# Optimization experiments

Hardware: AMD Instinct MI355X
Metric: run time of the kernel (lower is better)

The kernel has to match this reference:

```python
import jax, jax.numpy as jnp
import numpy as np

N_LAYERS = 4
D_MODEL = 64        # 8*8 hardcoded in source
D_STATE = 128
D_CONV = 4
EXPAND = 2
HEADDIM = 64        # Mamba2Simple default
D_INNER = EXPAND * D_MODEL            # 128
NHEADS = D_INNER // HEADDIM           # 2
NGROUPS = 1
D_IN_PROJ = 2 * D_INNER + 2 * NGROUPS * D_STATE + NHEADS   # 514
CONV_DIM = D_INNER + 2 * NGROUPS * D_STATE                 # 384
EPS = 1e-5
B_SZ, SEQ = 8, 4096


def setup_inputs() -> dict:
    key = jax.random.key(0)
    ks = jax.random.split(key, 8)
    s = 0.02
    x = jax.random.normal(ks[0], (B_SZ, SEQ, D_MODEL), jnp.float32)
    in_proj_w = jax.random.normal(ks[1], (N_LAYERS, D_IN_PROJ, D_MODEL), jnp.float32) * s
    conv_w = jax.random.normal(ks[2], (N_LAYERS, CONV_DIM, 1, D_CONV), jnp.float32) * 0.2
    conv_b = jnp.zeros((N_LAYERS, CONV_DIM), jnp.float32)
    # dt_bias ~ inverse-softplus of small dt values
    dt_bias = jax.random.uniform(ks[3], (N_LAYERS, NHEADS), jnp.float32, -4.0, 0.0)
    A_log = jnp.log(jax.random.uniform(ks[4], (N_LAYERS, NHEADS), jnp.float32, 1.0, 16.0))
    D = jnp.ones((N_LAYERS, NHEADS), jnp.float32)
    norm_w = jnp.ones((N_LAYERS, D_INNER), jnp.float32)
    out_proj_w = jax.random.normal(ks[5], (N_LAYERS, D_MODEL, D_INNER), jnp.float32) * s
    return {"x": x, "in_proj_w": in_proj_w, "conv_w": conv_w, "conv_b": conv_b,
            "dt_bias": dt_bias, "A_log": A_log, "D": D, "norm_w": norm_w,
            "out_proj_w": out_proj_w}


def _ssm(xh, dt, A, Bm, Cm):
    """Selective-scan SSM. xh:(B,L,H,P) dt:(B,L,H) A:(H,) Bm,Cm:(B,L,S) -> (B,L,H,P)"""
    dA = jnp.exp(dt * A)  # (B,L,H)

    def step(h, inp):
        dA_t, dt_t, x_t, B_t, C_t = inp
        # h: (B,H,P,S)
        h = h * dA_t[:, :, None, None] + (dt_t[:, :, None] * x_t)[..., None] * B_t[:, None, None, :]
        y = jnp.einsum('bhps,bs->bhp', h, C_t)
        return h, y

    b = xh.shape[0]
    h0 = jnp.zeros((b, NHEADS, HEADDIM, D_STATE), xh.dtype)
    xs = (jnp.moveaxis(dA, 1, 0), jnp.moveaxis(dt, 1, 0), jnp.moveaxis(xh, 1, 0),
          jnp.moveaxis(Bm, 1, 0), jnp.moveaxis(Cm, 1, 0))
    _, ys = jax.lax.scan(step, h0, xs)
    return jnp.moveaxis(ys, 0, 1)


def _layer(x, p):
    in_w, cw, cb, dtb, Alog, Dp, nw, ow = p
    zxbcdt = x @ in_w.T                                   # (B,L,514)
    z = zxbcdt[..., :D_INNER]
    xBC = zxbcdt[..., D_INNER:D_INNER + CONV_DIM]
    dt = jax.nn.softplus(zxbcdt[..., -NHEADS:] + dtb)     # (B,L,H)
    # causal depthwise conv over sequence
    xc = jnp.moveaxis(xBC, -1, 1)                         # (B,C,L)
    xc = jax.lax.conv_general_dilated(xc, cw, (1,), [(D_CONV - 1, 0)],
                                      dimension_numbers=('NCH', 'OIH', 'NCH'),
                                      feature_group_count=CONV_DIM)
    xBC = jax.nn.silu(jnp.moveaxis(xc + cb[None, :, None], 1, -1))
    xs = xBC[..., :D_INNER]
    Bm = xBC[..., D_INNER:D_INNER + D_STATE]
    Cm = xBC[..., D_INNER + D_STATE:]
    xh = xs.reshape(xs.shape[0], xs.shape[1], NHEADS, HEADDIM)
    A = -jnp.exp(Alog)                                    # (H,)
    y = _ssm(xh, dt, A, Bm, Cm) + Dp[None, None, :, None] * xh
    y = y.reshape(y.shape[0], y.shape[1], D_INNER)
    # gated RMSNorm (norm_before_gate=False): rmsnorm(y * silu(z)) * w
    y = y * jax.nn.silu(z)
    y = y * jax.lax.rsqrt(jnp.mean(y * y, axis=-1, keepdims=True) + EPS) * nw
    return y @ ow.T


def reference(x, in_proj_w, conv_w, conv_b, dt_bias, A_log, D, norm_w, out_proj_w):
    def body(xc, p):
        return _layer(xc, p) + xc, None
    out, _ = jax.lax.scan(body, x, (in_proj_w, conv_w, conv_b, dt_bias, A_log, D, norm_w, out_proj_w))
    return out
```

## Files before the change

kernel.cpp:

```cpp
#include <hip/hip_runtime.h>
#include <math.h>

#define B_SZ 8
#define SEQ  4096
#define DM   64
#define DI   128
#define NH   2
#define HD   64
#define DS   128
#define DIP  514
#define XW   384
#define CD   384
#define QC   64
#define NC   64
#define NR   (B_SZ*SEQ)
#define WPAD 576

typedef __attribute__((ext_vector_type(8))) short bf16x8;
typedef __attribute__((ext_vector_type(4))) float f32x4;

__device__ __forceinline__ unsigned short f2bf(float f) {
    union { float f; unsigned int u; } x; x.f = f;
    unsigned int r = x.u + 0x7fffu + ((x.u >> 16) & 1u);
    return (unsigned short)(r >> 16);
}
__device__ __forceinline__ float bf2f(unsigned short h) {
    union { unsigned int u; float f; } x; x.u = ((unsigned int)h) << 16;
    return x.f;
}
__device__ __forceinline__ bf16x8 fragld(const unsigned short* base, int r0, int k0, int ld) {
    int l = threadIdx.x & 63;
    return *(const bf16x8*)(base + (ptrdiff_t)(r0 + (l & 15)) * ld + k0 + (l >> 4) * 8);
}

__global__ __launch_bounds__(256) void k_wcvt(const float* __restrict__ in_w,
                                              const float* __restrict__ out_w,
                                              unsigned short* __restrict__ Wb,
                                              unsigned short* __restrict__ OWb) {
    int idx = blockIdx.x * 256 + threadIdx.x;
    if (idx < 4 * WPAD * 64) {
        int l = idx / (WPAD * 64), r = idx % (WPAD * 64);
        int n = r >> 6, k = r & 63;
        float v = (n < DIP) ? in_w[(size_t)l * DIP * 64 + (size_t)n * 64 + k] : 0.f;
        Wb[idx] = f2bf(v);
    }
    if (idx < 4 * 64 * 128) OWb[idx] = f2bf(out_w[idx]);
}

__global__ __launch_bounds__(256) void k_xcvt(const float* __restrict__ X,
                                              unsigned short* __restrict__ Xb) {
    int idx = (blockIdx.x * 256 + threadIdx.x) * 4;
    float4 v = *(const float4*)(X + idx);
    uint2 p;
    p.x = f2bf(v.x) | ((unsigned int)f2bf(v.y) << 16);
    p.y = f2bf(v.z) | ((unsigned int)f2bf(v.w) << 16);
    *(uint2*)(Xb + idx) = p;
}

__global__ __launch_bounds__(256) void k_inproj(const unsigned short* __restrict__ Xb,
                                                const unsigned short* __restrict__ Wb,
                                                unsigned short* __restrict__ ZXb,
                                                float* __restrict__ DT) {
    int m0 = blockIdx.x * 256;
    int ny = blockIdx.y;
    int tid = threadIdx.x;
    int wid = tid >> 6, lane = tid & 63;
    int q4 = lane >> 4, c16 = lane & 15;
    int mb = m0 + wid * 64;
    bf16x8 af[4][2];
#pragma unroll
    for (int mt = 0; mt < 4; mt++)
#pragma unroll
        for (int ks = 0; ks < 2; ks++)
            af[mt][ks] = *(const bf16x8*)(Xb + (size_t)(mb + mt * 16 + c16) * 64 + ks * 32 + q4 * 8);
    if (ny < 6) {
#pragma unroll
        for (int nt = 0; nt < 4; nt++) {
            bf16x8 bf[2];
#pragma unroll
            for (int ks = 0; ks < 2; ks++)
                bf[ks] = *(const bf16x8*)(Wb + (size_t)(128 + ny * 64 + nt * 16 + c16) * 64 + ks * 32 + q4 * 8);
#pragma unroll
            for (int mt = 0; mt < 4; mt++) {
                f32x4 acc = {0.f, 0.f, 0.f, 0.f};
                acc = __builtin_amdgcn_mfma_f32_16x16x32_bf16(af[mt][0], bf[0], acc, 0, 0, 0);
                acc = __builtin_amdgcn_mfma_f32_16x16x32_bf16(af[mt][1], bf[1], acc, 0, 0, 0);
#pragma unroll
                for (int rr = 0; rr < 4; rr++) {
                    float v = acc[rr];
                    float vn = __shfl_xor(v, 1);
                    if (!(lane & 1)) {
                        unsigned int pk = f2bf(v) | ((unsigned int)f2bf(vn) << 16);
                        *(unsigned int*)(ZXb + (size_t)(mb + mt * 16 + q4 * 4 + rr) * XW + ny * 64 + nt * 16 + c16) = pk;
                    }
                }
            }
        }
    } else {
        bf16x8 bf[2];
#pragma unroll
        for (int ks = 0; ks < 2; ks++)
            bf[ks] = *(const bf16x8*)(Wb + (size_t)(512 + c16) * 64 + ks * 32 + q4 * 8);
#pragma unroll
        for (int mt = 0; mt < 4; mt++) {
            f32x4 acc = {0.f, 0.f, 0.f, 0.f};
            acc = __builtin_amdgcn_mfma_f32_16x16x32_bf16(af[mt][0], bf[0], acc, 0, 0, 0);
            acc = __builtin_amdgcn_mfma_f32_16x16x32_bf16(af[mt][1], bf[1], acc, 0, 0, 0);
            if (c16 < 2)
#pragma unroll
                for (int rr = 0; rr < 4; rr++)
                    DT[(size_t)(mb + mt * 16 + q4 * 4 + rr) * 2 + c16] = acc[rr];
        }
    }
}

__global__ __launch_bounds__(1024, 8) void k_chunk1(
        const unsigned short* __restrict__ ZXb, const float* __restrict__ DT,
        const float* __restrict__ CW, const float* __restrict__ CB,
        const float* __restrict__ dtb, const float* __restrict__ Alog,
        const float* __restrict__ Dv,
        unsigned short* __restrict__ SL, unsigned short* __restrict__ CBuf,
        float* __restrict__ EB,
        float* __restrict__ TB, unsigned short* __restrict__ YBb) {
    __shared__ unsigned short sBt[128][72];
    __shared__ unsigned short sXt[128][72];
    __shared__ unsigned short uBC[2][64][136];
    __shared__ float s_cum[2][64], s_dt[2][64], s_w[2][64];
    unsigned short (*sM)[64][72] = (unsigned short (*)[64][72])&uBC[0][0][0];

    int c = blockIdx.x, b = blockIdx.y;
    size_t rbase = (size_t)b * SEQ + c * QC;
    int tid = threadIdx.x;
    int wid = tid >> 6, lane = tid & 63;
    int q4 = lane >> 4, c16 = lane & 15;

    if (wid < 2) {
        int h = wid, j = lane;
        float raw = DT[(rbase + j) * 2 + h] + dtb[h];
        float dt = (raw > 20.f) ? raw : log1pf(__expf(raw));
        float A = -__expf(Alog[h]);
        float x = dt * A;
        for (int off = 1; off < 64; off <<= 1) {
            float o = __shfl_up(x, off);
            if (lane >= off) x += o;
        }
        float T = __shfl(x, 63);
        s_dt[h][j] = dt;
        s_cum[h][j] = x;
        s_w[h][j] = __expf(T - x) * dt;
        EB[((size_t)(b * NC + c)) * 128 + h * 64 + j] = __expf(x);
        if (j == 0) TB[(b * 2 + h) * NC + c] = __expf(T);
    }

    size_t cbbase = ((size_t)(b * NC + c)) * 8192;
    for (int e = tid; e < 64 * 96; e += 1024) {
        int j = e / 96;
        int q = e - j * 96;
        int cc = q * 4;
        int l = c * QC + j;
        const unsigned short* zp = ZXb + (rbase + j) * XW + cc;
        uint2 a0 = *(const uint2*)zp;
        uint2 a1 = make_uint2(0, 0), a2 = make_uint2(0, 0), a3 = make_uint2(0, 0);
        if (l >= 1) a1 = *(const uint2*)(zp - XW);
        if (l >= 2) a2 = *(const uint2*)(zp - 2 * XW);
        if (l >= 3) a3 = *(const uint2*)(zp - 3 * XW);
        float v[4];
#pragma unroll
        for (int u = 0; u < 4; u++) {
            unsigned int w0 = (u < 2) ? a0.x : a0.y;
            unsigned int w1 = (u < 2) ? a1.x : a1.y;
            unsigned int w2 = (u < 2) ? a2.x : a2.y;
            unsigned int w3 = (u < 2) ? a3.x : a3.y;
            int sh = (u & 1) * 16;
            float r0 = bf2f((unsigned short)(w0 >> sh));
            float r1 = bf2f((unsigned short)(w1 >> sh));
            float r2 = bf2f((unsigned short)(w2 >> sh));
            float r3 = bf2f((unsigned short)(w3 >> sh));
            float4 wv = *(const float4*)(CW + (cc + u) * 4);
            float tt = CB[cc + u] + wv.w * r0 + wv.z * r1 + wv.y * r2 + wv.x * r3;
            v[u] = tt / (1.f + __expf(-tt));
        }
        if (cc < 128) {
#pragma unroll
            for (int u = 0; u < 4; u++) sXt[cc + u][j] = f2bf(v[u]);
        } else if (cc < 256) {
            int s = cc - 128;
            unsigned int p0 = f2bf(v[0]) | ((unsigned int)f2bf(v[1]) << 16);
            unsigned int p1 = f2bf(v[2]) | ((unsigned int)f2bf(v[3]) << 16);
            *(uint2*)&uBC[0][j][s] = make_uint2(p0, p1);
#pragma unroll
            for (int u = 0; u < 4; u++) sBt[s + u][j] = f2bf(v[u]);
        } else {
            int s = cc - 256;
            unsigned int p0 = f2bf(v[0]) | ((unsigned int)f2bf(v[1]) << 16);
            unsigned int p1 = f2bf(v[2]) | ((unsigned int)f2bf(v[3]) << 16);
            *(uint2*)&uBC[1][j][s] = make_uint2(p0, p1);
            *(uint2*)(CBuf + cbbase + (size_t)j * 128 + s) = make_uint2(p0, p1);
        }
    }
    __syncthreads();

    f32x4 gacc;
    {
        int it = wid >> 2, jt = wid & 3;
        f32x4 acc = {0.f, 0.f, 0.f, 0.f};
        for (int ks = 0; ks < 4; ks++) {
            bf16x8 a = fragld(&uBC[1][0][0], it * 16, ks * 32, 136);
            bf16x8 bb = fragld(&uBC[0][0][0], jt * 16, ks * 32, 136);
            acc = __builtin_amdgcn_mfma_f32_16x16x32_bf16(a, bb, acc, 0, 0, 0);
        }
        gacc = acc;
    }
    __syncthreads();
    {
        int it = wid >> 2, jt = wid & 3;
        int j = jt * 16 + c16;
        for (int rr = 0; rr < 4; rr++) {
            int i = it * 16 + q4 * 4 + rr;
            float gv = gacc[rr];
            for (int h = 0; h < 2; h++) {
                float m = 0.f;
                if (j <= i) m = gv * __expf(s_cum[h][i] - s_cum[h][j]) * s_dt[h][j];
                sM[h][i][j] = f2bf(m);
            }
        }
    }
    __syncthreads();

    size_t ybase = ((size_t)(b * NC + c)) * 8192;
#pragma unroll
    for (int u = 0; u < 2; u++) {
        int idx = wid * 2 + u;
        int h = idx >> 4, tt = idx & 15;
        int it = tt >> 2, pt = tt & 3;
        float dco = Dv[h];
        int pg = h * 64 + pt * 16 + c16;
        f32x4 acc;
        for (int rr = 0; rr < 4; rr++) {
            int i = it * 16 + q4 * 4 + rr;
            acc[rr] = dco * bf2f(sXt[pg][i]);
        }
        for (int ks = 0; ks < 2; ks++) {
            bf16x8 a = fragld(&sM[h][0][0], it * 16, ks * 32, 72);
            bf16x8 bb = fragld(&sXt[0][0], h * 64 + pt * 16, ks * 32, 72);
            acc = __builtin_amdgcn_mfma_f32_16x16x32_bf16(a, bb, acc, 0, 0, 0);
        }
        uint2 pk;
        pk.x = f2bf(acc[0]) | ((unsigned int)f2bf(acc[1]) << 16);
        pk.y = f2bf(acc[2]) | ((unsigned int)f2bf(acc[3]) << 16);
        *(uint2*)(YBb + ybase + (size_t)idx * 256 + lane * 4) = pk;
    }
    size_t slbase = ((size_t)(b * NC + c)) * 16384;
#pragma unroll
    for (int u = 0; u < 4; u++) {
        int idx = wid * 4 + u;
        int ptl = idx >> 3, st = idx & 7;
        int h = ptl >> 2;
        f32x4 acc = {0.f, 0.f, 0.f, 0.f};
        for (int ks = 0; ks < 2; ks++) {
            int jb = ks * 32 + (lane >> 4) * 8;
            bf16x8 a = fragld(&sXt[0][0], ptl * 16, ks * 32, 72);
            bf16x8 aw;
#pragma unroll
            for (int t = 0; t < 8; t++) aw[t] = (short)f2bf(bf2f((unsigned short)a[t]) * s_w[h][jb + t]);
            bf16x8 bb = fragld(&sBt[0][0], st * 16, ks * 32, 72);
            acc = __builtin_amdgcn_mfma_f32_16x16x32_bf16(aw, bb, acc, 0, 0, 0);
        }
        int s = st * 16 + c16;
        for (int rr = 0; rr < 4; rr++) {
            int p = ptl * 16 + q4 * 4 + rr;
            float vv = acc[rr];
            float vn = __shfl_xor(vv, 1);
            if (!(lane & 1)) {
                unsigned int pk = f2bf(vv) | ((unsigned int)f2bf(vn) << 16);
                *(unsigned int*)(SL + slbase + (size_t)p * 128 + s) = pk;
            }
        }
    }
}

__global__ __launch_bounds__(256) void k_scan(unsigned short* __restrict__ SL,
                                              const float* __restrict__ TB) {
    int bid = blockIdx.x;
    int b = bid >> 6;
    int ps = (bid & 63) * 256 + threadIdx.x;
    int h = ps >> 13;
    const float* dAp = TB + (b * 2 + h) * NC;
    size_t base = (size_t)(b * NC) * 16384 + ps;
    float hacc = 0.f;
#pragma unroll 8
    for (int cc = 0; cc < NC; cc++) {
        size_t idx = base + (size_t)cc * 16384;
        float slv = bf2f(SL[idx]);
        SL[idx] = f2bf(hacc);
        hacc = hacc * dAp[cc] + slv;
    }
}

__global__ __launch_bounds__(1024, 8) void k_fused(
        const unsigned short* __restrict__ SL, const unsigned short* __restrict__ CBuf,
        const float* __restrict__ EB,
        const unsigned short* __restrict__ YBb, const unsigned short* __restrict__ Wzb,
        const float* __restrict__ NW, const unsigned short* __restrict__ OWb,
        unsigned short* __restrict__ Xb, float* __restrict__ OutF,
        const unsigned short* __restrict__ WbN,
        unsigned short* __restrict__ ZXbO,
        float* __restrict__ DTO,
        int last) {
    __shared__ __attribute__((aligned(16))) unsigned short sH[128][136];
    __shared__ __attribute__((aligned(16))) unsigned short sE[128][136];
    float* sGf = (float*)&sH[0][0];
    unsigned short (*sG)[136] = (unsigned short (*)[136])&sE[0][0];
    unsigned short (*sX2)[72] = (unsigned short (*)[72])&sH[0][0];

    int c = blockIdx.x, b = blockIdx.y;
    size_t rbase = (size_t)b * SEQ + c * QC;
    int tid = threadIdx.x;
    int wid = tid >> 6, lane = tid & 63;
    size_t base = ((size_t)(b * NC + c)) * 16384;
    for (int u = 0; u < 2; u++) {
        int e = u * 1024 + tid;
        int row = e >> 4, cb8 = (e & 15) * 8;
        *(uint4*)&sH[row][cb8] = *(const uint4*)(SL + base + (size_t)row * 128 + cb8);
    }
    size_t cbbase = ((size_t)(b * NC + c)) * 8192;
    size_t ebase  = ((size_t)(b * NC + c)) * 128;
    {
        int i = tid >> 4, sc = (tid & 15) * 8;
        uint4 cv = *(const uint4*)(CBuf + cbbase + (size_t)i * 128 + sc);
        float e0 = EB[ebase + i], e1 = EB[ebase + 64 + i];
        unsigned int w[4] = {cv.x, cv.y, cv.z, cv.w};
        uint4 o0, o1;
        unsigned int* po0 = &o0.x;
        unsigned int* po1 = &o1.x;
#pragma unroll
        for (int t = 0; t < 4; t++) {
            float lo = bf2f((unsigned short)(w[t] & 0xffff));
            float hi = bf2f((unsigned short)(w[t] >> 16));
            po0[t] = f2bf(lo * e0) | ((unsigned int)f2bf(hi * e0) << 16);
            po1[t] = f2bf(lo * e1) | ((unsigned int)f2bf(hi * e1) << 16);
        }
        *(uint4*)&sE[i][sc] = o0;
        *(uint4*)&sE[64 + i][sc] = o1;
    }
    __syncthreads();
    int q4 = lane >> 4, c16 = lane & 15;

    float yv[2][4];
    int tit[2], tpg[2];
    size_t ybase = ((size_t)(b * NC + c)) * 8192;
#pragma unroll
    for (int u = 0; u < 2; u++) {
        int idx = wid * 2 + u;
        int h = idx >> 4, tt = idx & 15;
        int it = tt >> 2, pt = tt & 3;
        int pg = h * 64 + pt * 16 + c16;
        f32x4 zacc = {0.f, 0.f, 0.f, 0.f};
        f32x4 acc = {0.f, 0.f, 0.f, 0.f};
#pragma unroll
        for (int ks = 0; ks < 2; ks++) {
            bf16x8 xa = fragld(Xb, (int)rbase + it * 16, ks * 32, 64);
            bf16x8 wz = fragld(Wzb, h * 64 + pt * 16, ks * 32, 64);
            zacc = __builtin_amdgcn_mfma_f32_16x16x32_bf16(xa, wz, zacc, 0, 0, 0);
        }
        for (int ks = 0; ks < 4; ks++) {
            bf16x8 a = fragld(&sE[0][0], h * 64 + it * 16, ks * 32, 136);
            bf16x8 bb = fragld(&sH[0][0], h * 64 + pt * 16, ks * 32, 136);
            acc = __builtin_amdgcn_mfma_f32_16x16x32_bf16(a, bb, acc, 0, 0, 0);
        }
        tit[u] = it; tpg[u] = pg;
        uint2 yi = *(const uint2*)(YBb + ybase + (size_t)idx * 256 + lane * 4);
        float yin[4] = {bf2f((unsigned short)(yi.x & 0xffff)), bf2f((unsigned short)(yi.x >> 16)),
                        bf2f((unsigned short)(yi.y & 0xffff)), bf2f((unsigned short)(yi.y >> 16))};
        for (int rr = 0; rr < 4; rr++) {
            float y = acc[rr] + yin[rr];
            float z = zacc[rr];
            yv[u][rr] = y * (z / (1.f + __expf(-z)));
        }
    }
    __syncthreads();
#pragma unroll
    for (int u = 0; u < 2; u++)
        for (int rr = 0; rr < 4; rr++) {
            int i = tit[u] * 16 + q4 * 4 + rr;
            sGf[i * 132 + tpg[u]] = yv[u][rr];
        }
    __syncthreads();
    {
        int row = tid >> 4, part = tid & 15;
        int d0 = part * 8;
        float g[8];
        float ss = 0.f;
        for (int t2 = 0; t2 < 8; t2++) { g[t2] = sGf[row * 132 + d0 + t2]; ss += g[t2] * g[t2]; }
        ss += __shfl_xor(ss, 1);
        ss += __shfl_xor(ss, 2);
        ss += __shfl_xor(ss, 4);
        ss += __shfl_xor(ss, 8);
        float rms = rsqrtf(ss * (1.f / 128.f) + 1e-5f);
        for (int t2 = 0; t2 < 8; t2 += 2) {
            unsigned int pk = f2bf(g[t2] * rms * NW[d0 + t2]) |
                              ((unsigned int)f2bf(g[t2 + 1] * rms * NW[d0 + t2 + 1]) << 16);
            *(unsigned int*)&sG[row][d0 + t2] = pk;
        }
    }
    __syncthreads();
    {
        int mt = wid >> 2, nt = wid & 3;
        f32x4 acc = {0.f, 0.f, 0.f, 0.f};
        for (int ks = 0; ks < 4; ks++) {
            bf16x8 a = fragld(&sG[0][0], mt * 16, ks * 32, 136);
            bf16x8 bb = *(const bf16x8*)(OWb + (size_t)(nt * 16 + c16) * 128 + ks * 32 + q4 * 8);
            acc = __builtin_amdgcn_mfma_f32_16x16x32_bf16(a, bb, acc, 0, 0, 0);
        }
        for (int rr = 0; rr < 4; rr++) {
            int m = mt * 16 + q4 * 4 + rr;
            int n = nt * 16 + c16;
            size_t o = (rbase + m) * DM + n;
            float v = bf2f(Xb[o]) + acc[rr];
            if (last) {
                OutF[o] = v;
            } else {
                unsigned short vb = f2bf(v);
                sX2[m][n] = vb;
                float vn = __shfl_xor(v, 1);
                if (!(lane & 1)) {
                    unsigned int pk = (unsigned int)vb | ((unsigned int)f2bf(vn) << 16);
                    *(unsigned int*)(Xb + o) = pk;
                }
            }
        }
    }
    if (!last) {
        __syncthreads();
        for (int t = wid; t < 100; t += 16) {
            int mt2, n0;
            int isdt = (t >= 96);
            if (!isdt) { mt2 = t & 3; n0 = (t >> 2) * 16; }
            else       { mt2 = t - 96; n0 = 0; }
            bf16x8 a0 = fragld(&sX2[0][0], mt2 * 16, 0, 72);
            bf16x8 a1 = fragld(&sX2[0][0], mt2 * 16, 32, 72);
            const unsigned short* wrow = isdt ? (WbN + (size_t)(512 + c16) * 64)
                                              : (WbN + (size_t)(128 + n0 + c16) * 64);
            bf16x8 b0 = *(const bf16x8*)(wrow + q4 * 8);
            bf16x8 b1 = *(const bf16x8*)(wrow + 32 + q4 * 8);
            f32x4 acc = {0.f, 0.f, 0.f, 0.f};
            acc = __builtin_amdgcn_mfma_f32_16x16x32_bf16(a0, b0, acc, 0, 0, 0);
            acc = __builtin_amdgcn_mfma_f32_16x16x32_bf16(a1, b1, acc, 0, 0, 0);
            if (!isdt) {
#pragma unroll
                for (int rr = 0; rr < 4; rr++) {
                    float v = acc[rr];
                    float vn = __shfl_xor(v, 1);
                    if (!(lane & 1)) {
                        unsigned int pk = f2bf(v) | ((unsigned int)f2bf(vn) << 16);
                        *(unsigned int*)(ZXbO + (rbase + mt2 * 16 + q4 * 4 + rr) * XW + n0 + c16) = pk;
                    }
                }
            } else {
                if (c16 < 2)
#pragma unroll
                    for (int rr = 0; rr < 4; rr++)
                        DTO[(rbase + mt2 * 16 + q4 * 4 + rr) * 2 + c16] = acc[rr];
            }
        }
    }
}

extern "C" void kernel_launch(void* const* d_in, const int* in_sizes, int n_in,
                              void* d_out, int out_size, void* d_ws, size_t ws_size,
                              hipStream_t stream) {
    const float* x       = (const float*)d_in[0];
    const float* in_w    = (const float*)d_in[1];
    const float* conv_w  = (const float*)d_in[2];
    const float* conv_b  = (const float*)d_in[3];
    const float* dt_bias = (const float*)d_in[4];
    const float* A_log   = (const float*)d_in[5];
    const float* Dp      = (const float*)d_in[6];
    const float* norm_w  = (const float*)d_in[7];
    const float* out_w   = (const float*)d_in[8];
    float* out = (float*)d_out;
    float* ws  = (float*)d_ws;

    float* dt = ws;
    float* tb = dt + (size_t)NR * 2;
    float* eb = tb + 1024;
    unsigned short* zxb  = (unsigned short*)(eb + (size_t)B_SZ * NC * 128);
    unsigned short* ybb  = zxb + (size_t)NR * XW;
    unsigned short* sl   = ybb + (size_t)B_SZ * NC * 8192;
    unsigned short* cbuf = sl + (size_t)B_SZ * NC * 16384;
    unsigned short* xb   = cbuf + (size_t)B_SZ * NC * 8192;
    unsigned short* wb   = xb + (size_t)NR * DM;
    unsigned short* owb  = wb + (size_t)4 * WPAD * 64;

    k_wcvt<<<(4 * WPAD * 64 + 255) / 256, 256, 0, stream>>>(in_w, out_w, wb, owb);
    k_xcvt<<<NR * DM / 1024, 256, 0, stream>>>(x, xb);
    k_inproj<<<dim3(NR / 256, 7), 256, 0, stream>>>(xb, wb, zxb, dt);

    for (int layer = 0; layer < 4; layer++) {
        int nl = (layer < 3) ? layer + 1 : 3;
        k_chunk1<<<dim3(NC, B_SZ), 1024, 0, stream>>>(zxb, dt,
                conv_w + (size_t)layer * CD * 4, conv_b + (size_t)layer * CD,
                dt_bias + layer * NH, A_log + layer * NH, Dp + layer * NH,
                sl, cbuf, eb, tb, ybb);
        k_scan<<<512, 256, 0, stream>>>(sl, tb);
        k_fused<<<dim3(NC, B_SZ), 1024, 0, stream>>>(sl, cbuf, eb, ybb,
                wb + (size_t)layer * WPAD * 64, norm_w + layer * DI,
                owb + (size_t)layer * 64 * 128, xb, out,
                wb + (size_t)nl * WPAD * 64, zxb, dt,
                (layer == 3) ? 1 : 0);
    }
}
```

Measured before the change: 350.8 us.

## Use native bf16 conversions, pre-scale X in LDS, vectorize inter-chunk scan

```diff
diff --git a/kernel.cpp b/kernel.cpp
--- a/kernel.cpp
+++ b/kernel.cpp
@@ -18,11 +18,18 @@
 
 typedef __attribute__((ext_vector_type(8))) short bf16x8;
 typedef __attribute__((ext_vector_type(4))) float f32x4;
+typedef __attribute__((ext_vector_type(2))) __bf16 bf16x2;
 
 __device__ __forceinline__ unsigned short f2bf(float f) {
-    union { float f; unsigned int u; } x; x.f = f;
-    unsigned int r = x.u + 0x7fffu + ((x.u >> 16) & 1u);
-    return (unsigned short)(r >> 16);
+    union { __bf16 h; unsigned short u; } x;
+    x.h = (__bf16)f;
+    return x.u;
+}
+__device__ __forceinline__ unsigned int pk2(float lo, float hi) {
+    union { bf16x2 v; unsigned int u; } x;
+    x.v[0] = (__bf16)lo;
+    x.v[1] = (__bf16)hi;
+    return x.u;
 }
 __device__ __forceinline__ float bf2f(unsigned short h) {
     union { unsigned int u; float f; } x; x.u = ((unsigned int)h) << 16;
@@ -52,8 +59,8 @@
     int idx = (blockIdx.x * 256 + threadIdx.x) * 4;
     float4 v = *(const float4*)(X + idx);
     uint2 p;
-    p.x = f2bf(v.x) | ((unsigned int)f2bf(v.y) << 16);
-    p.y = f2bf(v.z) | ((unsigned int)f2bf(v.w) << 16);
+    p.x = pk2(v.x, v.y);
+    p.y = pk2(v.z, v.w);
     *(uint2*)(Xb + idx) = p;
 }
 
@@ -90,7 +97,7 @@
                     float v = acc[rr];
                     float vn = __shfl_xor(v, 1);
                     if (!(lane & 1)) {
-                        unsigned int pk = f2bf(v) | ((unsigned int)f2bf(vn) << 16);
+                        unsigned int pk = pk2(v, vn);
                         *(unsigned int*)(ZXb + (size_t)(mb + mt * 16 + q4 * 4 + rr) * XW + ny * 64 + nt * 16 + c16) = pk;
                     }
                 }
@@ -185,15 +192,15 @@
             for (int u = 0; u < 4; u++) sXt[cc + u][j] = f2bf(v[u]);
         } else if (cc < 256) {
             int s = cc - 128;
-            unsigned int p0 = f2bf(v[0]) | ((unsigned int)f2bf(v[1]) << 16);
-            unsigned int p1 = f2bf(v[2]) | ((unsigned int)f2bf(v[3]) << 16);
+            unsigned int p0 = pk2(v[0], v[1]);
+            unsigned int p1 = pk2(v[2], v[3]);
             *(uint2*)&uBC[0][j][s] = make_uint2(p0, p1);
 #pragma unroll
             for (int u = 0; u < 4; u++) sBt[s + u][j] = f2bf(v[u]);
         } else {
             int s = cc - 256;
-            unsigned int p0 = f2bf(v[0]) | ((unsigned int)f2bf(v[1]) << 16);
-            unsigned int p1 = f2bf(v[2]) | ((unsigned int)f2bf(v[3]) << 16);
+            unsigned int p0 = pk2(v[0], v[1]);
+            unsigned int p1 = pk2(v[2], v[3]);
             *(uint2*)&uBC[1][j][s] = make_uint2(p0, p1);
             *(uint2*)(CBuf + cbbase + (size_t)j * 128 + s) = make_uint2(p0, p1);
         }
@@ -246,25 +253,37 @@
             acc = __builtin_amdgcn_mfma_f32_16x16x32_bf16(a, bb, acc, 0, 0, 0);
         }
         uint2 pk;
-        pk.x = f2bf(acc[0]) | ((unsigned int)f2bf(acc[1]) << 16);
-        pk.y = f2bf(acc[2]) | ((unsigned int)f2bf(acc[3]) << 16);
+        pk.x = pk2(acc[0], acc[1]);
+        pk.y = pk2(acc[2], acc[3]);
         *(uint2*)(YBb + ybase + (size_t)idx * 256 + lane * 4) = pk;
     }
+    __syncthreads();
+    {
+        int row = tid >> 3, c0 = (tid & 7) * 8;
+        uint4 xv = *(uint4*)&sXt[row][c0];
+        const float* wp = s_w[row >> 6];
+        unsigned int* px = &xv.x;
+        uint4 ov;
+        unsigned int* po = &ov.x;
+#pragma unroll
+        for (int t = 0; t < 4; t++) {
+            float lo = bf2f((unsigned short)(px[t] & 0xffff)) * wp[c0 + 2 * t];
+            float hi = bf2f((unsigned short)(px[t] >> 16)) * wp[c0 + 2 * t + 1];
+            po[t] = pk2(lo, hi);
+        }
+        *(uint4*)&sXt[row][c0] = ov;
+    }
+    __syncthreads();
     size_t slbase = ((size_t)(b * NC + c)) * 16384;
 #pragma unroll
     for (int u = 0; u < 4; u++) {
         int idx = wid * 4 + u;
         int ptl = idx >> 3, st = idx & 7;
-        int h = ptl >> 2;
         f32x4 acc = {0.f, 0.f, 0.f, 0.f};
         for (int ks = 0; ks < 2; ks++) {
-            int jb = ks * 32 + (lane >> 4) * 8;
             bf16x8 a = fragld(&sXt[0][0], ptl * 16, ks * 32, 72);
-            bf16x8 aw;
-#pragma unroll
-            for (int t = 0; t < 8; t++) aw[t] = (short)f2bf(bf2f((unsigned short)a[t]) * s_w[h][jb + t]);
             bf16x8 bb = fragld(&sBt[0][0], st * 16, ks * 32, 72);
-            acc = __builtin_amdgcn_mfma_f32_16x16x32_bf16(aw, bb, acc, 0, 0, 0);
+            acc = __builtin_amdgcn_mfma_f32_16x16x32_bf16(a, bb, acc, 0, 0, 0);
         }
         int s = st * 16 + c16;
         for (int rr = 0; rr < 4; rr++) {
@@ -272,7 +291,7 @@
             float vv = acc[rr];
             float vn = __shfl_xor(vv, 1);
             if (!(lane & 1)) {
-                unsigned int pk = f2bf(vv) | ((unsigned int)f2bf(vn) << 16);
+                unsigned int pk = pk2(vv, vn);
                 *(unsigned int*)(SL + slbase + (size_t)p * 128 + s) = pk;
             }
         }
@@ -282,18 +301,22 @@
 __global__ __launch_bounds__(256) void k_scan(unsigned short* __restrict__ SL,
                                               const float* __restrict__ TB) {
     int bid = blockIdx.x;
-    int b = bid >> 6;
-    int ps = (bid & 63) * 256 + threadIdx.x;
-    int h = ps >> 13;
+    int b = bid >> 5;
+    int pu = (bid & 31) * 256 + threadIdx.x;
+    int h = pu >> 12;
     const float* dAp = TB + (b * 2 + h) * NC;
-    size_t base = (size_t)(b * NC) * 16384 + ps;
-    float hacc = 0.f;
+    size_t base = (size_t)(b * NC) * 16384 + (size_t)pu * 2;
+    float h0 = 0.f, h1 = 0.f;
 #pragma unroll 8
     for (int cc = 0; cc < NC; cc++) {
         size_t idx = base + (size_t)cc * 16384;
-        float slv = bf2f(SL[idx]);
-        SL[idx] = f2bf(hacc);
-        hacc = hacc * dAp[cc] + slv;
+        unsigned int v = *(unsigned int*)(SL + idx);
+        float s0 = bf2f((unsigned short)(v & 0xffff));
+        float s1 = bf2f((unsigned short)(v >> 16));
+        *(unsigned int*)(SL + idx) = pk2(h0, h1);
+        float dA = dAp[cc];
+        h0 = h0 * dA + s0;
+        h1 = h1 * dA + s1;
     }
 }
 
@@ -337,8 +360,8 @@
         for (int t = 0; t < 4; t++) {
             float lo = bf2f((unsigned short)(w[t] & 0xffff));
             float hi = bf2f((unsigned short)(w[t] >> 16));
-            po0[t] = f2bf(lo * e0) | ((unsigned int)f2bf(hi * e0) << 16);
-            po1[t] = f2bf(lo * e1) | ((unsigned int)f2bf(hi * e1) << 16);
+            po0[t] = pk2(lo * e0, hi * e0);
+            po1[t] = pk2(lo * e1, hi * e1);
         }
         *(uint4*)&sE[i][sc] = o0;
         *(uint4*)&sE[64 + i][sc] = o1;
@@ -398,8 +421,7 @@
         ss += __shfl_xor(ss, 8);
         float rms = rsqrtf(ss * (1.f / 128.f) + 1e-5f);
         for (int t2 = 0; t2 < 8; t2 += 2) {
-            unsigned int pk = f2bf(g[t2] * rms * NW[d0 + t2]) |
-                              ((unsigned int)f2bf(g[t2 + 1] * rms * NW[d0 + t2 + 1]) << 16);
+            unsigned int pk = pk2(g[t2] * rms * NW[d0 + t2], g[t2 + 1] * rms * NW[d0 + t2 + 1]);
             *(unsigned int*)&sG[row][d0 + t2] = pk;
         }
     }
@@ -452,7 +474,7 @@
                     float v = acc[rr];
                     float vn = __shfl_xor(v, 1);
                     if (!(lane & 1)) {
-                        unsigned int pk = f2bf(v) | ((unsigned int)f2bf(vn) << 16);
+                        unsigned int pk = pk2(v, vn);
                         *(unsigned int*)(ZXbO + (rbase + mt2 * 16 + q4 * 4 + rr) * XW + n0 + c16) = pk;
                     }
                 }
@@ -502,7 +524,7 @@
                 conv_w + (size_t)layer * CD * 4, conv_b + (size_t)layer * CD,
                 dt_bias + layer * NH, A_log + layer * NH, Dp + layer * NH,
                 sl, cbuf, eb, tb, ybb);
-        k_scan<<<512, 256, 0, stream>>>(sl, tb);
+        k_scan<<<256, 256, 0, stream>>>(sl, tb);
         k_fused<<<dim3(NC, B_SZ), 1024, 0, stream>>>(sl, cbuf, eb, ybb,
                 wb + (size_t)layer * WPAD * 64, norm_w + layer * DI,
                 owb + (size_t)layer * 64 * 128, xb, out,
```

Result: no change. 350.3 us (-0.1%).
